# Kernel optimization log

Measured on AMD Instinct MI355X. Metric: run time of the kernel, lower is better.

Reference implementation:

```python
import jax, jax.numpy as jnp
import numpy as np

N_EMBD = 512
N_HEAD = 8
N_INPUTS = 3
HEAD = N_EMBD // N_HEAD


def setup_inputs() -> dict:
    key = jax.random.key(0)
    ks = jax.random.split(key, 12)
    B, T1, T2, C, NI = 2, 2048, 2048, N_EMBD, N_INPUTS
    s = 0.02
    return {
        "x": jax.random.normal(ks[0], (B, T1, C), jnp.float32),
        "y": jax.random.normal(ks[1], (NI, B, T2, C), jnp.float32),
        "Wq": jax.random.normal(ks[2], (C, C), jnp.float32) * s,
        "bq": jnp.zeros((C,), jnp.float32),
        "Wk": jax.random.normal(ks[3], (NI, C, C), jnp.float32) * s,
        "bk": jnp.zeros((NI, C), jnp.float32),
        "Wv": jax.random.normal(ks[4], (NI, C, C), jnp.float32) * s,
        "bv": jnp.zeros((NI, C), jnp.float32),
        "Wp": jax.random.normal(ks[5], (C, C), jnp.float32) * s,
        "bp": jnp.zeros((C,), jnp.float32),
    }


def reference(x, y, Wq, bq, Wk, bk, Wv, bv, Wp, bp):
    B, T1, C = x.shape
    H, D = N_HEAD, HEAD
    # q: [B,H,T1,D], pre-scaled by 1/sqrt(D) as in the original
    q = (x @ Wq + bq).reshape(B, T1, H, D).transpose(0, 2, 1, 3)
    q = q / jnp.sqrt(jnp.asarray(D, q.dtype))
    out = jnp.zeros_like(q)
    for i in range(N_INPUTS):  # small fixed loop over distinct K/V sources
        yi = y[i]
        T2 = yi.shape[1]
        k = (yi @ Wk[i] + bk[i]).reshape(B, T2, H, D).transpose(0, 2, 1, 3)
        v = (yi @ Wv[i] + bv[i]).reshape(B, T2, H, D).transpose(0, 2, 1, 3)
        attn = jax.nn.softmax(jnp.einsum('bhqd,bhkd->bhqk', q, k), axis=-1)
        out = out + jnp.einsum('bhqk,bhkd->bhqd', attn, v)
    out = out.transpose(0, 2, 1, 3).reshape(B, T1, C)
    return out @ Wp + bp
```

## Files before the change

kernel.cpp:

```cpp
#include <hip/hip_runtime.h>

typedef __attribute__((ext_vector_type(8))) __bf16 bf16x8;
typedef __attribute__((ext_vector_type(4))) __bf16 bf16x4;
typedef __attribute__((ext_vector_type(4))) float f32x4;
typedef __attribute__((ext_vector_type(8))) unsigned short us8;

__device__ __forceinline__ unsigned short f2b(float f) {
    unsigned int u = __builtin_bit_cast(unsigned int, f);
    u = (u + 0x7fffu + ((u >> 16) & 1u)) >> 16;
    return (unsigned short)u;
}
__device__ __forceinline__ float b2f(unsigned short u) {
    return __builtin_bit_cast(float, (unsigned int)u << 16);
}
__device__ __forceinline__ void gload16(const void* g, void* l) {
    __builtin_amdgcn_global_load_lds(
        (const __attribute__((address_space(1))) unsigned int*)g,
        (__attribute__((address_space(3))) unsigned int*)l, 16, 0, 0);
}

__global__ void prep_w(const float* __restrict__ Wq, const float* __restrict__ Wk,
                       const float* __restrict__ Wv, const float* __restrict__ Wp,
                       unsigned short* __restrict__ Wt) {
    __shared__ float tile[64][65];
    int w = blockIdx.z;
    const float* src = (w == 0) ? Wq
                     : (w < 4)  ? Wk + (size_t)(w - 1) * 512 * 512
                     : (w < 7)  ? Wv + (size_t)(w - 4) * 512 * 512
                                : Wp;
    int n0 = blockIdx.x * 64, k0 = blockIdx.y * 64;
    int t = threadIdx.x;
    int rr = t >> 4, c4 = (t & 15) * 4;
#pragma unroll
    for (int j = 0; j < 4; j++) {
        int r = rr + j * 16;
        float4 v = *(const float4*)(src + (size_t)(k0 + r) * 512 + n0 + c4);
        tile[r][c4 + 0] = v.x; tile[r][c4 + 1] = v.y;
        tile[r][c4 + 2] = v.z; tile[r][c4 + 3] = v.w;
    }
    __syncthreads();
#pragma unroll
    for (int j = 0; j < 4; j++) {
        int rn = rr + j * 16;
        ushort4 o;
        o.x = f2b(tile[c4 + 0][rn]); o.y = f2b(tile[c4 + 1][rn]);
        o.z = f2b(tile[c4 + 2][rn]); o.w = f2b(tile[c4 + 3][rn]);
        *(ushort4*)(Wt + (size_t)w * 512 * 512 + (size_t)(n0 + rn) * 512 + k0 + c4) = o;
    }
}

template <int MODE>
__global__ __launch_bounds__(256, 4) void gemm_k(
    const float* __restrict__ x, const float* __restrict__ y,
    const unsigned short* __restrict__ Wt,
    const float* __restrict__ bq, const float* __restrict__ bk, const float* __restrict__ bv,
    unsigned short* __restrict__ Qb, unsigned short* __restrict__ Kb, unsigned short* __restrict__ Vb,
    const unsigned short* __restrict__ aob, const float* __restrict__ bp, float* __restrict__ outf) {
    __shared__ unsigned short As[128 * 64];
    __shared__ unsigned short Bs[128 * 64];

    const float* A = nullptr;
    const unsigned short* W;
    const float* bias;
    unsigned short* outb = nullptr;
    float scale = 1.f;
    if (MODE == 0) {
        int z = blockIdx.z;
        if (z == 0) {
            A = x; W = Wt; bias = bq; outb = Qb; scale = 0.125f;
        } else if (z < 4) {
            int i = z - 1;
            A = y + (size_t)i * 4096 * 512;
            W = Wt + (size_t)z * 512 * 512;
            bias = bk + i * 512;
            outb = Kb + (size_t)i * 4096 * 512;
        } else {
            int i = z - 4;
            A = y + (size_t)i * 4096 * 512;
            W = Wt + (size_t)z * 512 * 512;
            bias = bv + i * 512;
            outb = Vb + (size_t)i * 4096 * 512;
        }
    } else {
        W = Wt + (size_t)7 * 512 * 512; bias = bp;
    }

    int m0 = blockIdx.x * 128, n0 = blockIdx.y * 128;
    int t = threadIdx.x;
    int lane = t & 63, wid = t >> 6;
    int lg = lane >> 4, lr = lane & 15;
    int wm = wid >> 1, wn = wid & 1;
    int ssl = lane & 7, srow8 = lane >> 3;

    f32x4 acc[4][4];
    const f32x4 zf = {0.f, 0.f, 0.f, 0.f};
#pragma unroll
    for (int mi = 0; mi < 4; mi++)
#pragma unroll
        for (int ni = 0; ni < 4; ni++) acc[mi][ni] = zf;

    for (int kt = 0; kt < 8; ++kt) {
        __syncthreads();
#pragma unroll
        for (int j = 0; j < 4; j++) {
            int row = (j * 4 + wid) * 8 + srow8;
            gload16(W + (size_t)(n0 + row) * 512 + kt * 64 + ((ssl ^ (row & 7)) * 8),
                    Bs + (j * 4 + wid) * 512);
        }
        if (MODE == 0) {
#pragma unroll
            for (int j = 0; j < 8; j++) {
                int c = t + 256 * j;
                int row = c >> 4, kq = c & 15;
                float4 v = *(const float4*)(A + (size_t)(m0 + row) * 512 + kt * 64 + kq * 4);
                bf16x4 o4 = {(__bf16)v.x, (__bf16)v.y, (__bf16)v.z, (__bf16)v.w};
                *(bf16x4*)(As + row * 64 + (((kq >> 1) ^ (row & 7)) * 8) + (kq & 1) * 4) = o4;
            }
        } else {
#pragma unroll
            for (int j = 0; j < 4; j++) {
                int c = t + 256 * j;
                int row = c >> 3, sl = c & 7;
                const unsigned short* p0 = aob + (size_t)(m0 + row) * 512 + kt * 64 + sl * 8;
                us8 a0 = *(const us8*)p0;
                us8 a1 = *(const us8*)(p0 + (size_t)4096 * 512);
                us8 a2 = *(const us8*)(p0 + (size_t)2 * 4096 * 512);
                bf16x8 o8;
#pragma unroll
                for (int e = 0; e < 8; e++)
                    o8[e] = (__bf16)(b2f(a0[e]) + b2f(a1[e]) + b2f(a2[e]));
                *(bf16x8*)(As + row * 64 + ((sl ^ (row & 7)) * 8)) = o8;
            }
        }
        __syncthreads();

        bf16x8 af[4][2];
#pragma unroll
        for (int mi = 0; mi < 4; mi++)
#pragma unroll
            for (int kk = 0; kk < 2; kk++) {
                int row = wm * 64 + mi * 16 + lr;
                int sl = (kk * 4 + lg) ^ (row & 7);
                af[mi][kk] = *(const bf16x8*)(As + row * 64 + sl * 8);
            }
#pragma unroll
        for (int ni = 0; ni < 4; ni++)
#pragma unroll
            for (int kk = 0; kk < 2; kk++) {
                int row = wn * 64 + ni * 16 + lr;
                int sl = (kk * 4 + lg) ^ (row & 7);
                bf16x8 bf = *(const bf16x8*)(Bs + row * 64 + sl * 8);
#pragma unroll
                for (int mi = 0; mi < 4; mi++)
                    acc[mi][ni] = __builtin_amdgcn_mfma_f32_16x16x32_bf16(af[mi][kk], bf, acc[mi][ni], 0, 0, 0);
            }
    }

#pragma unroll
    for (int ni = 0; ni < 4; ni++) {
        int col = n0 + wn * 64 + ni * 16 + lr;
        float bb = bias[col];
#pragma unroll
        for (int mi = 0; mi < 4; mi++) {
            int row0 = m0 + wm * 64 + mi * 16 + lg * 4;
#pragma unroll
            for (int r = 0; r < 4; r++) {
                float v = (acc[mi][ni][r] + bb) * scale;
                if (MODE == 0)
                    outb[(size_t)(row0 + r) * 512 + col] = __builtin_bit_cast(unsigned short, (__bf16)v);
                else
                    outf[(size_t)(row0 + r) * 512 + col] = v;
            }
        }
    }
}

__global__ void transpose_v(const unsigned short* __restrict__ Vb,
                            unsigned short* __restrict__ Vt) {
    __shared__ unsigned short tile[64][68];
    int i = blockIdx.z, bh = blockIdx.y, t20 = blockIdx.x * 64;
    int b = bh >> 3, h = bh & 7;
    int t = threadIdx.x;
    int rr = t >> 4, c4 = (t & 15) * 4;
    const unsigned short* src = Vb + (size_t)i * 4096 * 512 + (size_t)(b * 2048 + t20) * 512 + h * 64;
#pragma unroll
    for (int j = 0; j < 4; j++) {
        int r = rr + j * 16;
        ushort4 v = *(const ushort4*)(src + (size_t)r * 512 + c4);
        tile[r][c4 + 0] = v.x; tile[r][c4 + 1] = v.y;
        tile[r][c4 + 2] = v.z; tile[r][c4 + 3] = v.w;
    }
    __syncthreads();
    unsigned short* dst = Vt + ((size_t)(i * 16 + bh) * 64) * 2048 + t20;
#pragma unroll
    for (int j = 0; j < 4; j++) {
        int d = rr + j * 16;
        ushort4 o;
        o.x = tile[c4 + 0][d]; o.y = tile[c4 + 1][d];
        o.z = tile[c4 + 2][d]; o.w = tile[c4 + 3][d];
        *(ushort4*)(dst + (size_t)d * 2048 + c4) = o;
    }
}

__global__ __launch_bounds__(256, 6) void attn_k(
    const unsigned short* __restrict__ Qb, const unsigned short* __restrict__ Kb,
    const unsigned short* __restrict__ Vt, unsigned short* __restrict__ attoutB) {
    __shared__ unsigned short Ks[64 * 64];
    __shared__ unsigned short Vs[64 * 64];
    __shared__ unsigned short Ps[4][16 * 64];

    int q0 = blockIdx.x * 64;
    int bh = blockIdx.y;
    int b = bh >> 3, h = bh & 7;
    int i = blockIdx.z;
    int t = threadIdx.x, lane = t & 63, wid = t >> 6;
    int lg = lane >> 4, lr = lane & 15;
    int ssl = lane & 7, srow = wid * 16 + (lane >> 3);
    int sswz = (ssl ^ (srow & 7)) * 8;

    const unsigned short* kb = Kb + ((size_t)i * 4096 + b * 2048) * 512 + h * 64;
    const unsigned short* vt = Vt + ((size_t)(i * 16 + bh) * 64) * 2048;

    const unsigned short* qp = Qb + (size_t)(b * 2048 + q0 + wid * 16 + lr) * 512 + h * 64 + lg * 8;
    bf16x8 qf0 = *(const bf16x8*)(qp);
    bf16x8 qf1 = *(const bf16x8*)(qp + 32);

    const f32x4 zf = {0.f, 0.f, 0.f, 0.f};
    f32x4 o[4];
#pragma unroll
    for (int ni = 0; ni < 4; ni++) o[ni] = zf;
    float m = -1e30f, l = 0.f;
    unsigned short* Pw = Ps[wid];

    for (int t20 = 0; t20 < 2048; t20 += 64) {
        __syncthreads();
        gload16(kb + (size_t)(t20 + srow) * 512 + sswz, Ks + (wid * 2 + 0) * 512);
        gload16(kb + (size_t)(t20 + srow + 8) * 512 + sswz, Ks + (wid * 2 + 1) * 512);
        gload16(vt + (size_t)srow * 2048 + t20 + sswz, Vs + (wid * 2 + 0) * 512);
        gload16(vt + (size_t)(srow + 8) * 2048 + t20 + sswz, Vs + (wid * 2 + 1) * 512);
        __syncthreads();

        f32x4 s[4];
#pragma unroll
        for (int ni = 0; ni < 4; ni++) s[ni] = zf;
        __builtin_amdgcn_s_setprio(1);
#pragma unroll
        for (int kk = 0; kk < 2; kk++) {
            bf16x8 q = kk ? qf1 : qf0;
#pragma unroll
            for (int ni = 0; ni < 4; ni++) {
                int row = ni * 16 + lr;
                int sl = (kk * 4 + lg) ^ (row & 7);
                bf16x8 kf = *(const bf16x8*)(Ks + row * 64 + sl * 8);
                s[ni] = __builtin_amdgcn_mfma_f32_16x16x32_bf16(kf, q, s[ni], 0, 0, 0);
            }
        }
        __builtin_amdgcn_s_setprio(0);

        float p0 = fmaxf(fmaxf(s[0][0], s[0][1]), fmaxf(s[0][2], s[0][3]));
        float p1 = fmaxf(fmaxf(s[1][0], s[1][1]), fmaxf(s[1][2], s[1][3]));
        float p2 = fmaxf(fmaxf(s[2][0], s[2][1]), fmaxf(s[2][2], s[2][3]));
        float p3 = fmaxf(fmaxf(s[3][0], s[3][1]), fmaxf(s[3][2], s[3][3]));
        float pmax = fmaxf(fmaxf(p0, p1), fmaxf(p2, p3));
        pmax = fmaxf(pmax, __shfl_xor(pmax, 16));
        pmax = fmaxf(pmax, __shfl_xor(pmax, 32));
        if (__any(pmax > m + 4.f)) {
            float mn = fmaxf(m, pmax);
            float fr = __expf(m - mn);
            l *= fr;
#pragma unroll
            for (int ni = 0; ni < 4; ni++)
#pragma unroll
                for (int r = 0; r < 4; r++) o[ni][r] *= fr;
            m = mn;
        }
        float lsum = 0.f;
#pragma unroll
        for (int ni = 0; ni < 4; ni++) {
            float e0 = __expf(s[ni][0] - m);
            float e1 = __expf(s[ni][1] - m);
            float e2 = __expf(s[ni][2] - m);
            float e3 = __expf(s[ni][3] - m);
            lsum += (e0 + e1) + (e2 + e3);
            bf16x4 pk = {(__bf16)e0, (__bf16)e1, (__bf16)e2, (__bf16)e3};
            *(bf16x4*)((char*)Pw + ((lr * 128 + ni * 32 + lg * 8) ^ ((lr & 7) << 4))) = pk;
        }
        lsum += __shfl_xor(lsum, 16);
        lsum += __shfl_xor(lsum, 32);
        l += lsum;

        asm volatile("s_waitcnt lgkmcnt(0)" ::: "memory");
        __builtin_amdgcn_sched_barrier(0);

        bf16x8 pa0 = *(const bf16x8*)((char*)Pw + ((lr * 128 + lg * 16) ^ ((lr & 7) << 4)));
        bf16x8 pa1 = *(const bf16x8*)((char*)Pw + ((lr * 128 + lg * 16 + 64) ^ ((lr & 7) << 4)));
        __builtin_amdgcn_s_setprio(1);
#pragma unroll
        for (int ni = 0; ni < 4; ni++) {
            int row = ni * 16 + lr;
            int sl0 = lg ^ (row & 7), sl1 = (4 + lg) ^ (row & 7);
            bf16x8 v0 = *(const bf16x8*)(Vs + row * 64 + sl0 * 8);
            bf16x8 v1 = *(const bf16x8*)(Vs + row * 64 + sl1 * 8);
            o[ni] = __builtin_amdgcn_mfma_f32_16x16x32_bf16(v0, pa0, o[ni], 0, 0, 0);
            o[ni] = __builtin_amdgcn_mfma_f32_16x16x32_bf16(v1, pa1, o[ni], 0, 0, 0);
        }
        __builtin_amdgcn_s_setprio(0);
    }

    float rl = 1.f / l;
    unsigned short* ao = attoutB + (size_t)i * 4096 * 512
                       + (size_t)(b * 2048 + q0 + wid * 16 + lr) * 512 + h * 64 + lg * 4;
#pragma unroll
    for (int ni = 0; ni < 4; ni++) {
        bf16x4 ov = {(__bf16)(o[ni][0] * rl), (__bf16)(o[ni][1] * rl),
                     (__bf16)(o[ni][2] * rl), (__bf16)(o[ni][3] * rl)};
        *(bf16x4*)(ao + ni * 16) = ov;
    }
}

extern "C" void kernel_launch(void* const* d_in, const int* in_sizes, int n_in,
                              void* d_out, int out_size, void* d_ws, size_t ws_size,
                              hipStream_t stream) {
    (void)in_sizes; (void)n_in; (void)out_size; (void)ws_size;
    const float* x  = (const float*)d_in[0];
    const float* y  = (const float*)d_in[1];
    const float* Wq = (const float*)d_in[2];
    const float* bq = (const float*)d_in[3];
    const float* Wk = (const float*)d_in[4];
    const float* bk = (const float*)d_in[5];
    const float* Wv = (const float*)d_in[6];
    const float* bv = (const float*)d_in[7];
    const float* Wp = (const float*)d_in[8];
    const float* bp = (const float*)d_in[9];
    float* out = (float*)d_out;

    char* ws = (char*)d_ws;
    const size_t MB = 1024 * 1024;
    unsigned short* Wt = (unsigned short*)(ws);
    unsigned short* Qb = (unsigned short*)(ws + 4 * MB);
    unsigned short* Kb = (unsigned short*)(ws + 8 * MB);
    unsigned short* Vb = (unsigned short*)(ws + 20 * MB);
    unsigned short* Vt = (unsigned short*)(ws + 32 * MB);
    unsigned short* attoutB = (unsigned short*)(ws + 20 * MB);

    prep_w<<<dim3(8, 8, 8), 256, 0, stream>>>(Wq, Wk, Wv, Wp, Wt);
    gemm_k<0><<<dim3(32, 4, 7), 256, 0, stream>>>(x, y, Wt, bq, bk, bv, Qb, Kb, Vb,
                                                  nullptr, nullptr, nullptr);
    transpose_v<<<dim3(32, 16, 3), 256, 0, stream>>>(Vb, Vt);
    attn_k<<<dim3(32, 16, 3), 256, 0, stream>>>(Qb, Kb, Vt, attoutB);
    gemm_k<1><<<dim3(32, 4, 1), 256, 0, stream>>>(nullptr, nullptr, Wt, nullptr, nullptr, nullptr,
                                                  nullptr, nullptr, nullptr, attoutB, bp, out);
}
```

Baseline: 259.2 us.

## Double-buffer attention K/V, use exp2 softmax, remap blocks per XCD, prefetch GEMM loads

The attention kernel now double-buffers K and V tiles in shared memory so the next tile loads while the current one computes. It folds log2(e) into the Q scale so softmax can use the native exp2, and it raises the lazy-rescale threshold. Both kernels switch to a 1D grid with an XCD-aware block remap, and the GEMM prefetches its fp32 A tile into registers before the barrier and raises MFMA priority. Occupancy hints are lowered to make room for the larger shared memory and register use.

```diff
diff --git a/kernel.cpp b/kernel.cpp
--- a/kernel.cpp
+++ b/kernel.cpp
@@ -13,11 +13,16 @@
 __device__ __forceinline__ float b2f(unsigned short u) {
     return __builtin_bit_cast(float, (unsigned int)u << 16);
 }
+__device__ __forceinline__ float exp2fast(float x) {
+    return __builtin_amdgcn_exp2f(x);
+}
 __device__ __forceinline__ void gload16(const void* g, void* l) {
     __builtin_amdgcn_global_load_lds(
         (const __attribute__((address_space(1))) unsigned int*)g,
         (__attribute__((address_space(3))) unsigned int*)l, 16, 0, 0);
 }
+
+#define LOG2E 1.44269504088896f
 
 __global__ void prep_w(const float* __restrict__ Wq, const float* __restrict__ Wk,
                        const float* __restrict__ Wv, const float* __restrict__ Wp,
@@ -50,7 +55,7 @@
 }
 
 template <int MODE>
-__global__ __launch_bounds__(256, 4) void gemm_k(
+__global__ __launch_bounds__(256, 3) void gemm_k(
     const float* __restrict__ x, const float* __restrict__ y,
     const unsigned short* __restrict__ Wt,
     const float* __restrict__ bq, const float* __restrict__ bk, const float* __restrict__ bv,
@@ -59,15 +64,26 @@
     __shared__ unsigned short As[128 * 64];
     __shared__ unsigned short Bs[128 * 64];
 
+    int bid = blockIdx.x;
+    int CHUNK = (MODE == 0) ? 112 : 16;
+    int w = (bid & 7) * CHUNK + (bid >> 3);
+    int z, mq, nq;
+    if (MODE == 0) {
+        z = w >> 7;
+        int rem = w & 127;
+        mq = rem >> 2; nq = rem & 3;
+    } else {
+        z = 0; mq = w >> 2; nq = w & 3;
+    }
+
     const float* A = nullptr;
     const unsigned short* W;
     const float* bias;
     unsigned short* outb = nullptr;
     float scale = 1.f;
     if (MODE == 0) {
-        int z = blockIdx.z;
         if (z == 0) {
-            A = x; W = Wt; bias = bq; outb = Qb; scale = 0.125f;
+            A = x; W = Wt; bias = bq; outb = Qb; scale = 0.125f * LOG2E;
         } else if (z < 4) {
             int i = z - 1;
             A = y + (size_t)i * 4096 * 512;
@@ -85,7 +101,7 @@
         W = Wt + (size_t)7 * 512 * 512; bias = bp;
     }
 
-    int m0 = blockIdx.x * 128, n0 = blockIdx.y * 128;
+    int m0 = mq * 128, n0 = nq * 128;
     int t = threadIdx.x;
     int lane = t & 63, wid = t >> 6;
     int lg = lane >> 4, lr = lane & 15;
@@ -100,6 +116,15 @@
         for (int ni = 0; ni < 4; ni++) acc[mi][ni] = zf;
 
     for (int kt = 0; kt < 8; ++kt) {
+        float4 av[8];
+        if (MODE == 0) {
+#pragma unroll
+            for (int j = 0; j < 8; j++) {
+                int c = t + 256 * j;
+                int row = c >> 4, kq = c & 15;
+                av[j] = *(const float4*)(A + (size_t)(m0 + row) * 512 + kt * 64 + kq * 4);
+            }
+        }
         __syncthreads();
 #pragma unroll
         for (int j = 0; j < 4; j++) {
@@ -112,7 +137,7 @@
             for (int j = 0; j < 8; j++) {
                 int c = t + 256 * j;
                 int row = c >> 4, kq = c & 15;
-                float4 v = *(const float4*)(A + (size_t)(m0 + row) * 512 + kt * 64 + kq * 4);
+                float4 v = av[j];
                 bf16x4 o4 = {(__bf16)v.x, (__bf16)v.y, (__bf16)v.z, (__bf16)v.w};
                 *(bf16x4*)(As + row * 64 + (((kq >> 1) ^ (row & 7)) * 8) + (kq & 1) * 4) = o4;
             }
@@ -143,6 +168,7 @@
                 int sl = (kk * 4 + lg) ^ (row & 7);
                 af[mi][kk] = *(const bf16x8*)(As + row * 64 + sl * 8);
             }
+        __builtin_amdgcn_s_setprio(1);
 #pragma unroll
         for (int ni = 0; ni < 4; ni++)
 #pragma unroll
@@ -154,6 +180,7 @@
                 for (int mi = 0; mi < 4; mi++)
                     acc[mi][ni] = __builtin_amdgcn_mfma_f32_16x16x32_bf16(af[mi][kk], bf, acc[mi][ni], 0, 0, 0);
             }
+        __builtin_amdgcn_s_setprio(0);
     }
 
 #pragma unroll
@@ -202,19 +229,22 @@
     }
 }
 
-__global__ __launch_bounds__(256, 6) void attn_k(
+__global__ __launch_bounds__(256, 4) void attn_k(
     const unsigned short* __restrict__ Qb, const unsigned short* __restrict__ Kb,
     const unsigned short* __restrict__ Vt, unsigned short* __restrict__ attoutB) {
-    __shared__ unsigned short Ks[64 * 64];
-    __shared__ unsigned short Vs[64 * 64];
+    __shared__ unsigned short Ks[2][64 * 64];
+    __shared__ unsigned short Vs[2][64 * 64];
     __shared__ unsigned short Ps[4][16 * 64];
 
-    int q0 = blockIdx.x * 64;
-    int bh = blockIdx.y;
+    int bid = blockIdx.x;
+    int w = (bid & 7) * 192 + (bid >> 3);
+    int q0 = (w & 31) * 64;
+    int bh = (w >> 5) & 15;
+    int i = w >> 9;
     int b = bh >> 3, h = bh & 7;
-    int i = blockIdx.z;
     int t = threadIdx.x, lane = t & 63, wid = t >> 6;
     int lg = lane >> 4, lr = lane & 15;
+    int x7 = lr & 7;
     int ssl = lane & 7, srow = wid * 16 + (lane >> 3);
     int sswz = (ssl ^ (srow & 7)) * 8;
 
@@ -225,20 +255,35 @@
     bf16x8 qf0 = *(const bf16x8*)(qp);
     bf16x8 qf1 = *(const bf16x8*)(qp + 32);
 
+    int fb0 = lr * 128 + ((lg ^ x7) << 4);
+    int fb1 = fb0 ^ 64;
+    int pwb = (lr * 128 + lg * 8) ^ (x7 << 4);
+    int prd0 = (lr * 128 + lg * 16) ^ (x7 << 4);
+    int prd1 = prd0 ^ 64;
+
     const f32x4 zf = {0.f, 0.f, 0.f, 0.f};
     f32x4 o[4];
 #pragma unroll
     for (int ni = 0; ni < 4; ni++) o[ni] = zf;
     float m = -1e30f, l = 0.f;
-    unsigned short* Pw = Ps[wid];
-
-    for (int t20 = 0; t20 < 2048; t20 += 64) {
+    char* Pw = (char*)Ps[wid];
+
+#define STAGE(buf, t20)                                                          \
+    do {                                                                         \
+        gload16(kb + (size_t)((t20) + srow) * 512 + sswz, Ks[buf] + (wid * 2 + 0) * 512);      \
+        gload16(kb + (size_t)((t20) + srow + 8) * 512 + sswz, Ks[buf] + (wid * 2 + 1) * 512);  \
+        gload16(vt + (size_t)srow * 2048 + (t20) + sswz, Vs[buf] + (wid * 2 + 0) * 512);       \
+        gload16(vt + (size_t)(srow + 8) * 2048 + (t20) + sswz, Vs[buf] + (wid * 2 + 1) * 512); \
+    } while (0)
+
+    STAGE(0, 0);
+    for (int tt = 0; tt < 32; tt++) {
+        int cur = tt & 1;
         __syncthreads();
-        gload16(kb + (size_t)(t20 + srow) * 512 + sswz, Ks + (wid * 2 + 0) * 512);
-        gload16(kb + (size_t)(t20 + srow + 8) * 512 + sswz, Ks + (wid * 2 + 1) * 512);
-        gload16(vt + (size_t)srow * 2048 + t20 + sswz, Vs + (wid * 2 + 0) * 512);
-        gload16(vt + (size_t)(srow + 8) * 2048 + t20 + sswz, Vs + (wid * 2 + 1) * 512);
-        __syncthreads();
+        if (tt + 1 < 32) STAGE(cur ^ 1, (tt + 1) * 64);
+
+        const char* Ksc = (const char*)Ks[cur];
+        const char* Vsc = (const char*)Vs[cur];
 
         f32x4 s[4];
 #pragma unroll
@@ -247,11 +292,10 @@
 #pragma unroll
         for (int kk = 0; kk < 2; kk++) {
             bf16x8 q = kk ? qf1 : qf0;
+            int fb = kk ? fb1 : fb0;
 #pragma unroll
             for (int ni = 0; ni < 4; ni++) {
-                int row = ni * 16 + lr;
-                int sl = (kk * 4 + lg) ^ (row & 7);
-                bf16x8 kf = *(const bf16x8*)(Ks + row * 64 + sl * 8);
+                bf16x8 kf = *(const bf16x8*)(Ksc + fb + ni * 2048);
                 s[ni] = __builtin_amdgcn_mfma_f32_16x16x32_bf16(kf, q, s[ni], 0, 0, 0);
             }
         }
@@ -264,9 +308,9 @@
         float pmax = fmaxf(fmaxf(p0, p1), fmaxf(p2, p3));
         pmax = fmaxf(pmax, __shfl_xor(pmax, 16));
         pmax = fmaxf(pmax, __shfl_xor(pmax, 32));
-        if (__any(pmax > m + 4.f)) {
+        if (__any(pmax > m + 6.f)) {
             float mn = fmaxf(m, pmax);
-            float fr = __expf(m - mn);
+            float fr = exp2fast(m - mn);
             l *= fr;
 #pragma unroll
             for (int ni = 0; ni < 4; ni++)
@@ -277,13 +321,13 @@
         float lsum = 0.f;
 #pragma unroll
         for (int ni = 0; ni < 4; ni++) {
-            float e0 = __expf(s[ni][0] - m);
-            float e1 = __expf(s[ni][1] - m);
-            float e2 = __expf(s[ni][2] - m);
-            float e3 = __expf(s[ni][3] - m);
+            float e0 = exp2fast(s[ni][0] - m);
+            float e1 = exp2fast(s[ni][1] - m);
+            float e2 = exp2fast(s[ni][2] - m);
+            float e3 = exp2fast(s[ni][3] - m);
             lsum += (e0 + e1) + (e2 + e3);
             bf16x4 pk = {(__bf16)e0, (__bf16)e1, (__bf16)e2, (__bf16)e3};
-            *(bf16x4*)((char*)Pw + ((lr * 128 + ni * 32 + lg * 8) ^ ((lr & 7) << 4))) = pk;
+            *(bf16x4*)(Pw + (pwb ^ (ni * 32))) = pk;
         }
         lsum += __shfl_xor(lsum, 16);
         lsum += __shfl_xor(lsum, 32);
@@ -292,20 +336,19 @@
         asm volatile("s_waitcnt lgkmcnt(0)" ::: "memory");
         __builtin_amdgcn_sched_barrier(0);
 
-        bf16x8 pa0 = *(const bf16x8*)((char*)Pw + ((lr * 128 + lg * 16) ^ ((lr & 7) << 4)));
-        bf16x8 pa1 = *(const bf16x8*)((char*)Pw + ((lr * 128 + lg * 16 + 64) ^ ((lr & 7) << 4)));
+        bf16x8 pa0 = *(const bf16x8*)(Pw + prd0);
+        bf16x8 pa1 = *(const bf16x8*)(Pw + prd1);
         __builtin_amdgcn_s_setprio(1);
 #pragma unroll
         for (int ni = 0; ni < 4; ni++) {
-            int row = ni * 16 + lr;
-            int sl0 = lg ^ (row & 7), sl1 = (4 + lg) ^ (row & 7);
-            bf16x8 v0 = *(const bf16x8*)(Vs + row * 64 + sl0 * 8);
-            bf16x8 v1 = *(const bf16x8*)(Vs + row * 64 + sl1 * 8);
+            bf16x8 v0 = *(const bf16x8*)(Vsc + fb0 + ni * 2048);
+            bf16x8 v1 = *(const bf16x8*)(Vsc + fb1 + ni * 2048);
             o[ni] = __builtin_amdgcn_mfma_f32_16x16x32_bf16(v0, pa0, o[ni], 0, 0, 0);
             o[ni] = __builtin_amdgcn_mfma_f32_16x16x32_bf16(v1, pa1, o[ni], 0, 0, 0);
         }
         __builtin_amdgcn_s_setprio(0);
     }
+#undef STAGE
 
     float rl = 1.f / l;
     unsigned short* ao = attoutB + (size_t)i * 4096 * 512
@@ -344,10 +387,10 @@
     unsigned short* attoutB = (unsigned short*)(ws + 20 * MB);
 
     prep_w<<<dim3(8, 8, 8), 256, 0, stream>>>(Wq, Wk, Wv, Wp, Wt);
-    gemm_k<0><<<dim3(32, 4, 7), 256, 0, stream>>>(x, y, Wt, bq, bk, bv, Qb, Kb, Vb,
-                                                  nullptr, nullptr, nullptr);
+    gemm_k<0><<<896, 256, 0, stream>>>(x, y, Wt, bq, bk, bv, Qb, Kb, Vb,
+                                       nullptr, nullptr, nullptr);
     transpose_v<<<dim3(32, 16, 3), 256, 0, stream>>>(Vb, Vt);
-    attn_k<<<dim3(32, 16, 3), 256, 0, stream>>>(Qb, Kb, Vt, attoutB);
-    gemm_k<1><<<dim3(32, 4, 1), 256, 0, stream>>>(nullptr, nullptr, Wt, nullptr, nullptr, nullptr,
-                                                  nullptr, nullptr, nullptr, attoutB, bp, out);
-}
+    attn_k<<<1536, 256, 0, stream>>>(Qb, Kb, Vt, attoutB);
+    gemm_k<1><<<128, 256, 0, stream>>>(nullptr, nullptr, Wt, nullptr, nullptr, nullptr,
+                                       nullptr, nullptr, nullptr, attoutB, bp, out);
+}
```

Measured after the change: 235.6 us. 9.1% less time.
